# Kernel optimization log

Measured on AMD Instinct MI355X. Metric: run time of the kernel, lower is better.

## Reference

```python
import jax, jax.numpy as jnp
import numpy as np

B, N, D, K = 4, 4096, 1024, 256
AMPLITUDE_MAX = 3.0
GATE_BIAS = float(np.log(0.65 / 0.35))  # logit(gate_bias_init=0.65)


def setup_inputs() -> dict:
    key = jax.random.key(0)
    k0, k1, k2 = jax.random.split(key, 3)
    return {
        "x": jax.random.normal(k0, (B, N, D), jnp.float32),
        "W_proj": jax.random.normal(k1, (6 * K, D), jnp.float32) * (1.0 / np.sqrt(D)),
        "b_proj": jnp.zeros((6 * K,), jnp.float32),
        "W_res": jax.random.normal(k2, (D, 2 * K), jnp.float32) * 0.002,
        "res_scale": jnp.float32(0.05),
    }


def _resonance_scan(alpha, drive_r, drive_i):
    """r_t = alpha_t * r_{t-1} + v_t, associative prefix scan over seq axis=1."""
    b = jnp.stack([drive_r, drive_i], axis=-1)      # (B, N, K, 2)
    a = alpha[..., None]                            # (B, N, K, 1)

    def combine(left, right):
        a_l, b_l = left
        a_r, b_r = right
        return (a_l * a_r, a_r * b_l + b_r)

    _, r = jax.lax.associative_scan(combine, (a, b), axis=1)
    return r[..., 0], r[..., 1]                     # (B, N, K) each


def reference(x, W_proj, b_proj, W_res, res_scale):
    n = x.shape[1]
    # OscillatorProjection: one fused linear -> 6 heads of size K
    raw = jnp.einsum('bnd,pd->bnp', x, W_proj) + b_proj        # (B, n, 6K)
    A_raw, o_raw, phi, al_raw, g_raw, be_raw = jnp.split(raw, 6, axis=-1)
    A = AMPLITUDE_MAX * jax.nn.sigmoid(A_raw)                  # amplitude in (0, amplitude_max)
    omega = jax.nn.softplus(o_raw)                             # positive frequency
    alpha = jax.nn.sigmoid(al_raw + GATE_BIAS)                 # decay gate, fp32
    g_out = jax.nn.sigmoid(g_raw)
    beta = jax.nn.sigmoid(be_raw)

    # phase_mode == 'log' positions
    pos = jnp.log1p(jnp.arange(n, dtype=jnp.float32))[None, :, None]
    angle = omega * pos + phi
    cos_a = jnp.cos(angle)
    sin_a = jnp.sin(angle)

    one_m_a = 1.0 - alpha
    drive_r = one_m_a * A * cos_a
    drive_i = one_m_a * A * sin_a

    r_r, r_i = _resonance_scan(alpha, drive_r, drive_i)

    # forget-gate erase along current phase direction
    readout = r_r * cos_a + r_i * sin_a
    r_r = r_r - beta * readout * cos_a
    r_i = r_i - beta * readout * sin_a

    # state norm: r /= max(|r|, 1.0)
    modulus = jnp.sqrt(r_r * r_r + r_i * r_i + 1e-8)
    scale = jnp.maximum(modulus, 1.0)
    r_r = r_r / scale
    r_i = r_i / scale

    # demodulate: rho = r * exp(-j*angle)
    rho_re = r_r * cos_a + r_i * sin_a
    rho_im = -r_r * sin_a + r_i * cos_a
    rho = jnp.concatenate([g_out * rho_re, g_out * rho_im], axis=-1)  # (B, n, 2K)

    # eval mode: warmup_factor = 1.0
    return res_scale * jnp.einsum('bnk,dk->bnd', rho, W_res)
```

## Files before the change

### kernel.cpp

```cpp
#include <hip/hip_runtime.h>
#include <hip/hip_bf16.h>
#include <cstdint>
#include <cstddef>

#define B_ 4
#define N_ 4096
#define D_ 1024
#define K_ 256
#define M_ (B_ * N_)
#define P_ (6 * K_)
#define DK2_ (2 * K_)

static __device__ __forceinline__ float sigm(float x) {
    return 1.0f / (1.0f + __expf(-x));
}
static __device__ __forceinline__ float softplusf_(float x) {
    return fmaxf(x, 0.0f) + __logf(1.0f + __expf(-fabsf(x)));
}
static __device__ __forceinline__ unsigned short f2bf(float f) {
    uint32_t u = __float_as_uint(f);
    uint32_t r = (u + 0x7FFFu + ((u >> 16) & 1u)) >> 16;
    return (unsigned short)r;
}

#define GATE_BIAS 0.6190392084062235f
#define AMP_MAX 3.0f

typedef __attribute__((ext_vector_type(8))) __bf16 bf16x8;
typedef __attribute__((ext_vector_type(4))) float f32x4;

static __device__ __forceinline__ void gload_lds16(const unsigned short* g, unsigned short* l) {
    __builtin_amdgcn_global_load_lds(
        (const __attribute__((address_space(1))) void*)g,
        (__attribute__((address_space(3))) void*)l, 16, 0, 0);
}

__global__ __launch_bounds__(256) void cvt_kernel(const float* __restrict__ src,
                                                  unsigned short* __restrict__ dst, int n4) {
    int i = blockIdx.x * 256 + threadIdx.x;
    if (i < n4) {
        float4 v = reinterpret_cast<const float4*>(src)[i];
        ushort4 o;
        o.x = f2bf(v.x); o.y = f2bf(v.y); o.z = f2bf(v.z); o.w = f2bf(v.w);
        reinterpret_cast<ushort4*>(dst)[i] = o;
    }
}


#define FRAG(BUF, r, kc) \
    (*reinterpret_cast<const bf16x8*>(&(BUF)[(size_t)(r) * 64 + (((((kc) >> 3) ^ ((r) & 7)) << 3))]))

template <int BN, bool ADD_BIAS, bool SCALE, typename OutT>
__global__ __launch_bounds__(512, 2) void gemm_bt(const unsigned short* __restrict__ A,
                                                  const unsigned short* __restrict__ Bm,
                                                  const float* __restrict__ bias,
                                                  const float* __restrict__ scale_p,
                                                  OutT* __restrict__ C, int M, int N, int Kd) {
    constexpr int NB = BN / 64;
    constexpr int WCOL = BN / 4;
    __shared__ unsigned short As0[256 * 64];
    __shared__ unsigned short Bs0[BN * 64];
    __shared__ unsigned short As1[256 * 64];
    __shared__ unsigned short Bs1[BN * 64];

    const int tid = threadIdx.x;
    const int w = tid >> 6, l = tid & 63;
    const int m0 = blockIdx.x * 256;
    const int n0 = blockIdx.y * BN;
    const int wm = w >> 2, wn = w & 3;
    const int lr = l & 15, lk = (l >> 4) * 8;
    const int nt = Kd >> 6;

    const int srow = tid >> 3;
    const int sslot = tid & 7;
    const int wbase = tid & ~63;

    f32x4 acc[8][NB];
#pragma unroll
    for (int mi = 0; mi < 8; ++mi)
#pragma unroll
        for (int ni = 0; ni < NB; ++ni) acc[mi][ni] = (f32x4){0.f, 0.f, 0.f, 0.f};

#define STAGE_GROUP(SRC, DST, ROW0G, K0, G)                                           \
    {                                                                                 \
        int row = (G) * 64 + srow;                                                    \
        int col = (K0) + ((sslot ^ (srow & 7)) << 3);                                 \
        gload_lds16((SRC) + (size_t)((ROW0G) + row) * Kd + col,                       \
                    (DST) + (size_t)((((G) * 512 + wbase)) * 8));                     \
    }

#define PHASE(CA, CB, KK, MIH, STAGE_CODE, TAIL_CODE)                                 \
    {                                                                                 \
        _Pragma("unroll") for (int f = 0; f < 4; ++f) {                               \
            int ar = wm * 128 + ((MIH) * 4 + f) * 16 + lr;                            \
            af[f] = FRAG(CA, ar, (KK) + lk);                                          \
        }                                                                             \
        if ((MIH) == 0) {                                                             \
            _Pragma("unroll") for (int f = 0; f < NB; ++f) {                          \
                int br = wn * WCOL + f * 16 + lr;                                     \
                bfr[f] = FRAG(CB, br, (KK) + lk);                                     \
            }                                                                         \
        }                                                                             \
        STAGE_CODE;                                                                   \
        __builtin_amdgcn_s_setprio(1);                                                \
        _Pragma("unroll") for (int mi = 0; mi < 4; ++mi)                              \
            _Pragma("unroll") for (int ni = 0; ni < NB; ++ni)                         \
                acc[(MIH) * 4 + mi][ni] = __builtin_amdgcn_mfma_f32_16x16x32_bf16(    \
                    af[mi], bfr[ni], acc[(MIH) * 4 + mi][ni], 0, 0, 0);               \
        __builtin_amdgcn_s_setprio(0);                                                \
        TAIL_CODE;                                                                    \
        __builtin_amdgcn_s_barrier();                                                 \
    }

#define TILE_STEP(T, CA, CB, PA, PB)                                                  \
    {                                                                                 \
        const int knext = ((T) + 1) * 64;                                             \
        const bool do_stage = ((T) + 1 < nt);                                         \
        bf16x8 af[4], bfr[NB];                                                        \
        PHASE(CA, CB, 0, 0,                                                           \
              if (do_stage) {                                                         \
                  _Pragma("unroll") for (int g = 0; g < 4; ++g)                       \
                      STAGE_GROUP(A, PA, m0, knext, g);                               \
                  _Pragma("unroll") for (int g = 0; g < NB; ++g)                      \
                      STAGE_GROUP(Bm, PB, n0, knext, g);                              \
              },                                                                      \
              {});                                                                    \
        PHASE(CA, CB, 0, 1, {}, {});                                                  \
        PHASE(CA, CB, 32, 0, {}, {});                                                 \
        PHASE(CA, CB, 32, 1, {},                                                      \
              asm volatile("s_waitcnt vmcnt(0)" ::: "memory"));                       \
    }

#pragma unroll
    for (int g = 0; g < 4; ++g) STAGE_GROUP(A, As0, m0, 0, g);
#pragma unroll
    for (int g = 0; g < NB; ++g) STAGE_GROUP(Bm, Bs0, n0, 0, g);
    asm volatile("s_waitcnt vmcnt(0)" ::: "memory");
    __builtin_amdgcn_s_barrier();

    for (int t = 0; t < nt; t += 2) {
        TILE_STEP(t, As0, Bs0, As1, Bs1);
        TILE_STEP(t + 1, As1, Bs1, As0, Bs0);
    }

    float sc = SCALE ? *scale_p : 1.0f;
#pragma unroll
    for (int mi = 0; mi < 8; ++mi) {
        int row = m0 + wm * 128 + mi * 16 + (l >> 4) * 4;
#pragma unroll
        for (int ni = 0; ni < NB; ++ni) {
            int col = n0 + wn * WCOL + ni * 16 + lr;
            float bv = ADD_BIAS ? bias[col] : 0.0f;
#pragma unroll
            for (int j = 0; j < 4; ++j) {
                float v = acc[mi][ni][j] + bv;
                if (SCALE) v *= sc;
                C[(size_t)(row + j) * N + col] = (OutT)v;
            }
        }
    }
#undef STAGE_GROUP
#undef PHASE
#undef TILE_STEP
}

struct Step {
    float alpha, dr, di, cs, sn, g, beta;
};
template <bool FULL>
static __device__ __forceinline__ Step compute_step(const _Float16* __restrict__ p, float pos) {
    Step s;
    float a_raw = (float)p[0];
    float o_raw = (float)p[K_];
    float phi   = (float)p[2 * K_];
    float al    = (float)p[3 * K_];
    float A     = AMP_MAX * sigm(a_raw);
    float omega = softplusf_(o_raw);
    float alpha = sigm(al + GATE_BIAS);
    float angle = omega * pos + phi;
    float sn, cs;
    __sincosf(angle, &sn, &cs);
    float oma = 1.0f - alpha;
    s.alpha = alpha;
    s.dr = oma * A * cs;
    s.di = oma * A * sn;
    s.cs = cs;
    s.sn = sn;
    if (FULL) {
        s.g    = sigm((float)p[4 * K_]);
        s.beta = sigm((float)p[5 * K_]);
    }
    return s;
}

__global__ __launch_bounds__(256) void scan_sum_kernel(const _Float16* __restrict__ raw,
                                                       float* __restrict__ sA,
                                                       float* __restrict__ sR,
                                                       float* __restrict__ sI,
                                                       float* __restrict__ subA,
                                                       float* __restrict__ subR,
                                                       float* __restrict__ subI) {
    const int tid = threadIdx.x;
    const int c = tid & 15, t = tid >> 4;
    const int chunk = blockIdx.x, kg = blockIdx.y, b = blockIdx.z;
    const int k = kg * 16 + c;
    const int n0 = chunk * 256 + t * 16;
    const _Float16* base = raw + (size_t)(b * N_ + n0) * P_ + k;

    float aP = 1.0f, rR = 0.0f, rI = 0.0f;
#pragma unroll
    for (int j = 0; j < 16; ++j) {
        Step s = compute_step<false>(base + (size_t)j * P_, __logf((float)(n0 + j + 1)));
        aP *= s.alpha;
        rR = s.alpha * rR + s.dr;
        rI = s.alpha * rI + s.di;
    }
    const int chan = b * K_ + kg * 16 + c;
    const int sidx = (chunk * 16 + t) * 1024 + chan;
    subA[sidx] = aP;
    subR[sidx] = rR;
    subI[sidx] = rI;

    __shared__ float lA[256], lR[256], lI[256];
    lA[c * 16 + t] = aP;
    lR[c * 16 + t] = rR;
    lI[c * 16 + t] = rI;
    __syncthreads();
    if (tid < 16) {
        float a = 1.0f, r = 0.0f, im = 0.0f;
        for (int tt = 0; tt < 16; ++tt) {
            float at = lA[tid * 16 + tt];
            r  = at * r  + lR[tid * 16 + tt];
            im = at * im + lI[tid * 16 + tt];
            a *= at;
        }
        int chanw = b * K_ + kg * 16 + tid;
        sA[chunk * 1024 + chanw] = a;
        sR[chunk * 1024 + chanw] = r;
        sI[chunk * 1024 + chanw] = im;
    }
}

__global__ __launch_bounds__(256) void scan_apply_kernel(const _Float16* __restrict__ raw,
                                                         const float* __restrict__ sA,
                                                         const float* __restrict__ sR,
                                                         const float* __restrict__ sI,
                                                         const float* __restrict__ subA,
                                                         const float* __restrict__ subR,
                                                         const float* __restrict__ subI,
                                                         unsigned short* __restrict__ rho) {
    const int tid = threadIdx.x;
    const int c = tid & 15, t = tid >> 4;
    const int chunk = blockIdx.x, kg = blockIdx.y, b = blockIdx.z;
    const int k = kg * 16 + c;
    const int n0 = chunk * 256 + t * 16;
    const _Float16* base = raw + (size_t)(b * N_ + n0) * P_ + k;

    float pR = 0.0f, pI = 0.0f;
    if (tid < 16) {
        int chan = b * K_ + kg * 16 + tid;
        for (int ch = 0; ch < chunk; ++ch) {
            float a = sA[ch * 1024 + chan];
            pR = a * pR + sR[ch * 1024 + chan];
            pI = a * pI + sI[ch * 1024 + chan];
        }
    }
    __shared__ float lA[256], lR[256], lI[256], pTR[256], pTI[256];
    {
        const int chan = b * K_ + kg * 16 + c;
        const int sidx = (chunk * 16 + t) * 1024 + chan;
        lA[c * 16 + t] = subA[sidx];
        lR[c * 16 + t] = subR[sidx];
        lI[c * 16 + t] = subI[sidx];
    }
    __syncthreads();
    if (tid < 16) {
        float r = pR, im = pI;
        for (int tt = 0; tt < 16; ++tt) {
            pTR[tid * 16 + tt] = r;
            pTI[tid * 16 + tt] = im;
            float at = lA[tid * 16 + tt];
            r  = at * r  + lR[tid * 16 + tt];
            im = at * im + lI[tid * 16 + tt];
        }
    }
    __syncthreads();
    float r = pTR[c * 16 + t], im = pTI[c * 16 + t];
    unsigned short* orow = rho + (size_t)(b * N_ + n0) * DK2_ + k;
#pragma unroll
    for (int j = 0; j < 16; ++j) {
        Step s = compute_step<true>(base + (size_t)j * P_, __logf((float)(n0 + j + 1)));
        r  = s.alpha * r  + s.dr;
        im = s.alpha * im + s.di;
        float readout = r * s.cs + im * s.sn;
        float r2 = r  - s.beta * readout * s.cs;
        float i3 = im - s.beta * readout * s.sn;
        float mod = __fsqrt_rn(r2 * r2 + i3 * i3 + 1e-8f);
        float scl = fmaxf(mod, 1.0f);
        float inv = 1.0f / scl;
        float rr = r2 * inv, ri = i3 * inv;
        float rho_re = rr * s.cs + ri * s.sn;
        float rho_im = -rr * s.sn + ri * s.cs;
        orow[(size_t)j * DK2_]      = f2bf(s.g * rho_re);
        orow[(size_t)j * DK2_ + K_] = f2bf(s.g * rho_im);
    }
}

extern "C" void kernel_launch(void* const* d_in, const int* in_sizes, int n_in,
                              void* d_out, int out_size, void* d_ws, size_t ws_size,
                              hipStream_t stream) {
    const float* x  = (const float*)d_in[0];
    const float* Wp = (const float*)d_in[1];
    const float* bp = (const float*)d_in[2];
    const float* Wr = (const float*)d_in[3];
    const float* rs = (const float*)d_in[4];
    float* out = (float*)d_out;
    char* ws = (char*)d_ws;

    _Float16* raw = (_Float16*)ws;
    unsigned short* xb  = (unsigned short*)(ws + 100663296);
    unsigned short* wpb = (unsigned short*)(ws + 134217728);
    unsigned short* wrb = (unsigned short*)(ws + 137363456);
    float* sA = (float*)(ws + 138412032);
    float* sR = (float*)(ws + 138477568);
    float* sI = (float*)(ws + 138543104);
    unsigned short* rho = xb;
    float* subA = (float*)(ws + 134217728);
    float* subR = (float*)(ws + 135266304);
    float* subI = (float*)(ws + 136314880);

    cvt_kernel<<<16384, 256, 0, stream>>>(x, xb, M_ * D_ / 4);
    cvt_kernel<<<1536, 256, 0, stream>>>(Wp, wpb, P_ * D_ / 4);
    cvt_kernel<<<512, 256, 0, stream>>>(Wr, wrb, D_ * DK2_ / 4);

    gemm_bt<192, true, false, _Float16><<<dim3(M_ / 256, P_ / 192), 512, 0, stream>>>(
        xb, wpb, bp, nullptr, raw, M_, P_, D_);

    scan_sum_kernel<<<dim3(16, 16, 4), 256, 0, stream>>>(raw, sA, sR, sI, subA, subR, subI);
    scan_apply_kernel<<<dim3(16, 16, 4), 256, 0, stream>>>(raw, sA, sR, sI, subA, subR, subI, rho);

    gemm_bt<256, false, true, float><<<dim3(M_ / 256, D_ / 256), 512, 0, stream>>>(
        rho, wrb, nullptr, rs, out, M_, D_, DK2_);
}
```

Before: 140.8 us.

## Spread next-tile global-to-LDS staging across GEMM phases with partial vmcnt waits

The GEMM main loop used to issue every global-to-LDS load for the next K tile in the first phase and wait for all of them at the end. It now spreads the B and A stage groups across the four MFMA phases and waits with vmcnt(2), so only the groups the next phase needs must have landed. Each phase gains an extra barrier and an lgkmcnt wait before its MFMAs. The goal is smoother memory issue and more overlap with compute, at the cost of more barriers and fragile hand-counted wait ordering.

```diff
diff --git a/kernel.cpp b/kernel.cpp
--- a/kernel.cpp
+++ b/kernel.cpp
@@ -81,66 +81,88 @@
 #pragma unroll
         for (int ni = 0; ni < NB; ++ni) acc[mi][ni] = (f32x4){0.f, 0.f, 0.f, 0.f};
 
-#define STAGE_GROUP(SRC, DST, ROW0G, K0, G)                                           \
+#define STAGE_A(PA, K0, G)                                                            \
     {                                                                                 \
         int row = (G) * 64 + srow;                                                    \
         int col = (K0) + ((sslot ^ (srow & 7)) << 3);                                 \
-        gload_lds16((SRC) + (size_t)((ROW0G) + row) * Kd + col,                       \
-                    (DST) + (size_t)((((G) * 512 + wbase)) * 8));                     \
-    }
-
-#define PHASE(CA, CB, KK, MIH, STAGE_CODE, TAIL_CODE)                                 \
+        gload_lds16(A + (size_t)(m0 + row) * Kd + col, (PA) + ((G) * 512 + wbase) * 8); \
+    }
+#define STAGE_B(PB, K0, G)                                                            \
+    {                                                                                 \
+        int row = (G) * 64 + srow;                                                    \
+        int col = (K0) + ((sslot ^ (srow & 7)) << 3);                                 \
+        gload_lds16(Bm + (size_t)(n0 + row) * Kd + col, (PB) + ((G) * 512 + wbase) * 8); \
+    }
+
+#define PH_BAR \
+    __builtin_amdgcn_s_barrier(); \
+    asm volatile("" ::: "memory");
+
+#define PHASE(CA, CB, KK, MIH, READB, STAGES, WCODE)                                  \
     {                                                                                 \
         _Pragma("unroll") for (int f = 0; f < 4; ++f) {                               \
             int ar = wm * 128 + ((MIH) * 4 + f) * 16 + lr;                            \
             af[f] = FRAG(CA, ar, (KK) + lk);                                          \
         }                                                                             \
-        if ((MIH) == 0) {                                                             \
+        if (READB) {                                                                  \
             _Pragma("unroll") for (int f = 0; f < NB; ++f) {                          \
                 int br = wn * WCOL + f * 16 + lr;                                     \
                 bfr[f] = FRAG(CB, br, (KK) + lk);                                     \
             }                                                                         \
         }                                                                             \
-        STAGE_CODE;                                                                   \
+        STAGES;                                                                       \
+        WCODE;                                                                        \
+        PH_BAR;                                                                       \
+        asm volatile("s_waitcnt lgkmcnt(0)" ::: "memory");                            \
         __builtin_amdgcn_s_setprio(1);                                                \
         _Pragma("unroll") for (int mi = 0; mi < 4; ++mi)                              \
             _Pragma("unroll") for (int ni = 0; ni < NB; ++ni)                         \
                 acc[(MIH) * 4 + mi][ni] = __builtin_amdgcn_mfma_f32_16x16x32_bf16(    \
                     af[mi], bfr[ni], acc[(MIH) * 4 + mi][ni], 0, 0, 0);               \
         __builtin_amdgcn_s_setprio(0);                                                \
-        TAIL_CODE;                                                                    \
-        __builtin_amdgcn_s_barrier();                                                 \
-    }
-
-#define TILE_STEP(T, CA, CB, PA, PB)                                                  \
+        PH_BAR;                                                                       \
+    }
+
+#define TILE(T, CA, CB, PA, PB)                                                       \
     {                                                                                 \
-        const int knext = ((T) + 1) * 64;                                             \
-        const bool do_stage = ((T) + 1 < nt);                                         \
+        const int kn = ((T) + 1) * 64;                                                \
+        const bool ds = ((T) + 1 < nt);                                               \
         bf16x8 af[4], bfr[NB];                                                        \
-        PHASE(CA, CB, 0, 0,                                                           \
-              if (do_stage) {                                                         \
-                  _Pragma("unroll") for (int g = 0; g < 4; ++g)                       \
-                      STAGE_GROUP(A, PA, m0, knext, g);                               \
-                  _Pragma("unroll") for (int g = 0; g < NB; ++g)                      \
-                      STAGE_GROUP(Bm, PB, n0, knext, g);                              \
-              },                                                                      \
-              {});                                                                    \
-        PHASE(CA, CB, 0, 1, {}, {});                                                  \
-        PHASE(CA, CB, 32, 0, {}, {});                                                 \
-        PHASE(CA, CB, 32, 1, {},                                                      \
-              asm volatile("s_waitcnt vmcnt(0)" ::: "memory"));                       \
-    }
-
-#pragma unroll
-    for (int g = 0; g < 4; ++g) STAGE_GROUP(A, As0, m0, 0, g);
-#pragma unroll
-    for (int g = 0; g < NB; ++g) STAGE_GROUP(Bm, Bs0, n0, 0, g);
-    asm volatile("s_waitcnt vmcnt(0)" ::: "memory");
-    __builtin_amdgcn_s_barrier();
+        PHASE(CA, CB, 0, 0, true,                                                     \
+              { if (ds) { STAGE_B(PB, kn, 0); STAGE_B(PB, kn, 1); } },                \
+              { if (ds) asm volatile("s_waitcnt vmcnt(2)" ::: "memory");              \
+                else    asm volatile("s_waitcnt vmcnt(0)" ::: "memory"); });          \
+        PHASE(CA, CB, 0, 1, false,                                                    \
+              { if (ds) {                                                             \
+                    if constexpr (NB == 3) { STAGE_B(PB, kn, 2); STAGE_A(PA, kn, 0); }\
+                    else { STAGE_B(PB, kn, 2); STAGE_B(PB, kn, 3); }                  \
+                } }, {});                                                             \
+        PHASE(CA, CB, 32, 0, true,                                                    \
+              { if (ds) {                                                             \
+                    if constexpr (NB == 3) { STAGE_A(PA, kn, 2); STAGE_A(PA, kn, 1);  \
+                                             STAGE_A(PA, kn, 3); }                    \
+                    else { STAGE_A(PA, kn, 0); STAGE_A(PA, kn, 2); }                  \
+                } }, {});                                                             \
+        PHASE(CA, CB, 32, 1, false,                                                   \
+              { if (ds) {                                                             \
+                    if constexpr (NB == 4) { STAGE_A(PA, kn, 1); STAGE_A(PA, kn, 3); }\
+                } },                                                                  \
+              { if (ds) asm volatile("s_waitcnt vmcnt(2)" ::: "memory"); });          \
+    }
+
+    if constexpr (NB == 3) {
+        STAGE_B(Bs0, 0, 0); STAGE_B(Bs0, 0, 1); STAGE_B(Bs0, 0, 2);
+        STAGE_A(As0, 0, 0); STAGE_A(As0, 0, 2); STAGE_A(As0, 0, 1); STAGE_A(As0, 0, 3);
+    } else {
+        STAGE_B(Bs0, 0, 0); STAGE_B(Bs0, 0, 1); STAGE_B(Bs0, 0, 2); STAGE_B(Bs0, 0, 3);
+        STAGE_A(As0, 0, 0); STAGE_A(As0, 0, 2); STAGE_A(As0, 0, 1); STAGE_A(As0, 0, 3);
+    }
+    asm volatile("s_waitcnt vmcnt(2)" ::: "memory");
+    PH_BAR;
 
     for (int t = 0; t < nt; t += 2) {
-        TILE_STEP(t, As0, Bs0, As1, Bs1);
-        TILE_STEP(t + 1, As1, Bs1, As0, Bs0);
+        TILE(t, As0, Bs0, As1, Bs1);
+        TILE(t + 1, As1, Bs1, As0, Bs0);
     }
 
     float sc = SCALE ? *scale_p : 1.0f;
@@ -159,9 +181,11 @@
             }
         }
     }
-#undef STAGE_GROUP
+#undef STAGE_A
+#undef STAGE_B
+#undef PH_BAR
 #undef PHASE
-#undef TILE_STEP
+#undef TILE
 }
 
 struct Step {
```

After: 144.0 us. 2.3% more time.
